# Kernel optimization log

Hardware: AMD Instinct MI355X
Metric: run time of the kernel (lower is better)

The kernel has to match this reference:

```python
import jax, jax.numpy as jnp
import numpy as np


def setup_inputs() -> dict:
    key = jax.random.key(0)
    ks = jax.random.split(key, 7)
    C = 256
    Cqk = C // 8  # 32
    B, D, H, W = 4, 16, 16, 16
    s_in = 1.0 / np.sqrt(C)  # conv1x1 fan_in = C
    return {
        "x": jax.random.normal(ks[0], (B, C, D, H, W), dtype=jnp.float32),
        "Wq": jax.random.uniform(ks[1], (Cqk, C), jnp.float32, -s_in, s_in),
        "bq": jax.random.uniform(ks[2], (Cqk,), jnp.float32, -s_in, s_in),
        "Wk": jax.random.uniform(ks[3], (Cqk, C), jnp.float32, -s_in, s_in),
        "bk": jax.random.uniform(ks[4], (Cqk,), jnp.float32, -s_in, s_in),
        "Wv": jax.random.uniform(ks[5], (C, C), jnp.float32, -s_in, s_in),
        "bv": jax.random.uniform(ks[6], (C,), jnp.float32, -s_in, s_in),
    }


def reference(x, Wq, bq, Wk, bk, Wv, bv):
    B, C, D, H, W = x.shape
    N = D * H * W
    xf = x.reshape(B, C, N)  # [B, C, N]
    # 1x1x1 convs == per-voxel GEMMs over the channel dim
    q = jnp.einsum('oc,bcn->bon', Wq, xf) + bq[None, :, None]  # [B, Cqk, N]
    k = jnp.einsum('oc,bcn->bon', Wk, xf) + bk[None, :, None]  # [B, Cqk, N]
    v = jnp.einsum('oc,bcn->bon', Wv, xf) + bv[None, :, None]  # [B, C, N]
    # attention[b, n, m] = softmax_m( q[:, n] . k[:, m] )
    scores = jnp.einsum('bcn,bcm->bnm', q, k)  # [B, N, N]
    attn = jax.nn.softmax(scores, axis=-1)
    # out = value @ attention^T  -> out[b, c, n] = sum_m v[b,c,m] * attn[b,n,m]
    out = jnp.einsum('bcm,bnm->bcn', v, attn)
    return x + out.reshape(B, C, D, H, W)
```

## Files before the change

### kernel.cpp

```cpp
#include <hip/hip_runtime.h>
#include <math.h>

#define B_   4
#define C_   256
#define CQK  32
#define N_   4096
#define TQ   64
#define TM   64
#define HITERS ((N_ / 2) / TM)
#define PSS  72
#define XT2  264
#define VOS  40

typedef __attribute__((ext_vector_type(8))) short short8;
typedef __attribute__((ext_vector_type(4))) short short4v;
typedef __attribute__((ext_vector_type(4))) float f32x4;
typedef __attribute__((ext_vector_type(2))) unsigned int uint2v;

#if __has_builtin(__builtin_amdgcn_exp2f)
#define EXP2F(x) __builtin_amdgcn_exp2f(x)
#else
#define EXP2F(x) exp2f(x)
#endif

__device__ __forceinline__ unsigned short f2bf(float f) {
    unsigned u = __builtin_bit_cast(unsigned, f);
    u += 0x7fffu + ((u >> 16) & 1u);
    return (unsigned short)(u >> 16);
}
__device__ __forceinline__ float bf2f(unsigned short s) {
    return __builtin_bit_cast(float, (unsigned)s << 16);
}
__device__ __forceinline__ unsigned pack2bf(float a, float b) {
    unsigned ua = __builtin_bit_cast(unsigned, a) + 0x8000u;
    unsigned ub = __builtin_bit_cast(unsigned, b) + 0x8000u;
#if __has_builtin(__builtin_amdgcn_perm)
    return __builtin_amdgcn_perm(ub, ua, 0x07060302u);
#else
    return (ua >> 16) | (ub & 0xffff0000u);
#endif
}

__global__ __launch_bounds__(256) void cvt_w(
    const float* __restrict__ Wq, const float* __restrict__ bq,
    const float* __restrict__ Wk, const float* __restrict__ bk,
    const float* __restrict__ Wv, const float* __restrict__ bv,
    unsigned short* __restrict__ wbf, float* __restrict__ biasf)
{
    const float LOG2E = 1.4426950408889634f;
    const int r = blockIdx.x;
    const int t = threadIdx.x;
    const float* src = (r < 32) ? (Wq + r * C_)
                     : (r < 64) ? (Wk + (r - 32) * C_)
                                : (Wv + (r - 64) * C_);
    const float scale = (r < 32) ? LOG2E : 1.0f;
    wbf[r * C_ + t] = f2bf(src[t] * scale);
    if (t == 0)
        biasf[r] = (r < 32) ? bq[r] * LOG2E : (r < 64) ? bk[r - 32] : bv[r - 64];
}

__global__ __launch_bounds__(256, 2) void proj_qkv(
    const float* __restrict__ x, const unsigned short* __restrict__ wbf,
    const float* __restrict__ biasf,
    unsigned short* __restrict__ qb, unsigned short* __restrict__ kb,
    unsigned short* __restrict__ vb)
{
    __shared__ __align__(16) unsigned short xT[32 * XT2];
    __shared__ __align__(16) unsigned short vout[256 * VOS];
    __shared__ __align__(16) unsigned short qks[32 * 72];

    const int t    = threadIdx.x;
    const int w    = t >> 6;
    const int lane = t & 63;
    const int quad = lane >> 4;
    const int c16  = lane & 15;
    const int n0   = blockIdx.x * 32;
    const int b    = blockIdx.y;

    {
        const int c0 = (t >> 3) * 8;
        const int nq = t & 7;
        f32x4 xv[8];
#pragma unroll
        for (int i = 0; i < 8; ++i)
            xv[i] = *(const f32x4*)&x[((size_t)(b * C_) + c0 + i) * N_ + n0 + 4 * nq];
#pragma unroll
        for (int j = 0; j < 4; ++j) {
            short8 pk;
#pragma unroll
            for (int i = 0; i < 8; ++i) pk[i] = (short)f2bf(xv[i][j]);
            *(short8*)&xT[(4 * nq + j) * XT2 + c0] = pk;
        }
    }
    __syncthreads();

    f32x4 acc[5][2];
#pragma unroll
    for (int i = 0; i < 5; ++i)
#pragma unroll
        for (int nt = 0; nt < 2; ++nt) acc[i][nt] = (f32x4){0.f, 0.f, 0.f, 0.f};

    const unsigned short* wr = wbf + (size_t)(80 * w + c16) * C_ + quad * 8;

#pragma unroll
    for (int ks = 0; ks < 8; ++ks) {
        short8 af[5], bf[2];
#pragma unroll
        for (int i = 0; i < 5; ++i)
            af[i] = *(const short8*)(wr + (size_t)(16 * i) * C_ + 32 * ks);
#pragma unroll
        for (int nt = 0; nt < 2; ++nt)
            bf[nt] = *(const short8*)&xT[(16 * nt + c16) * XT2 + ks * 32 + quad * 8];
#pragma unroll
        for (int i = 0; i < 5; ++i)
#pragma unroll
            for (int nt = 0; nt < 2; ++nt)
                acc[i][nt] = __builtin_amdgcn_mfma_f32_16x16x32_bf16(af[i], bf[nt], acc[i][nt], 0, 0, 0);
    }

#pragma unroll
    for (int i = 0; i < 5; ++i) {
        const int OT = 5 * w + i;
        const int obase = OT * 16 + 4 * quad;
        const f32x4 bv4 = *(const f32x4*)&biasf[obase];
#pragma unroll
        for (int nt = 0; nt < 2; ++nt) {
            const int n = 16 * nt + c16;
            float vals[4];
#pragma unroll
            for (int r = 0; r < 4; ++r) vals[r] = acc[i][nt][r] + bv4[r];
            if (OT >= 4) {
#pragma unroll
                for (int r = 0; r < 4; ++r)
                    vout[(obase + r - 64) * VOS + n] = f2bf(vals[r]);
            } else {
                const int col = (OT < 2 ? 0 : 32) + (OT & 1) * 16 + 4 * quad;
                short4v pk;
#pragma unroll
                for (int r = 0; r < 4; ++r) pk[r] = (short)f2bf(vals[r]);
                *(short4v*)&qks[n * 72 + col] = pk;
            }
        }
    }
    __syncthreads();

#pragma unroll
    for (int p = 0; p < 4; ++p) {
        const int c   = 64 * p + (t >> 2);
        const int seg = t & 3;
        const short8 vv = *(const short8*)&vout[c * VOS + seg * 8];
        *(short8*)(vb + ((size_t)(b * C_) + c) * N_ + n0 + seg * 8) = vv;
    }
    if (w < 2) {
        unsigned short* dst = w ? kb : qb;
        const int coff = w ? 32 : 0;
#pragma unroll
        for (int h = 0; h < 2; ++h) {
            const int n = 16 * h + (lane >> 2);
            const int c = (lane & 3) * 8;
            const short8 v = *(const short8*)&qks[n * 72 + coff + c];
            *(short8*)(dst + ((size_t)(b * N_) + n0 + n) * 32 + c) = v;
        }
    }
}

__global__ __launch_bounds__(512, 4) void attn_kernel(
    const unsigned short* __restrict__ qg,
    const unsigned short* __restrict__ kg,
    const unsigned short* __restrict__ vg,
    float* __restrict__ outp,
    unsigned short* __restrict__ Op1,
    float* __restrict__ lp)
{
    __shared__ __align__(16) unsigned short ks[TM * 40];
    __shared__ __align__(16) unsigned short vs[C_ * TM];
    __shared__ __align__(16) unsigned short ps[TQ * PSS];
    __shared__ float ls[4 * TQ];

    const int t    = threadIdx.x;
    const int w    = t >> 6;
    const int lane = t & 63;
    const int quad = lane >> 4;
    const int c16  = lane & 15;
    const int flat = blockIdx.x;
    const int half = flat & 1;
    const int b    = (flat >> 1) & 3;
    const int q0   = (flat >> 3) * TQ;
    const int kvb0 = half * (N_ / 2);
    const int f   = w & 3;
    const int qg_ = w >> 2;
    const int cs = w & 3;
    const int pg = w >> 2;

    const unsigned short* kbase = kg + (size_t)(b * N_) * 32;
    const unsigned short* vbase = vg + (size_t)(b * C_) * N_;

    short8 bq[2];
#pragma unroll
    for (int g = 0; g < 2; ++g)
        bq[g] = *(const short8*)(qg + ((size_t)(b * N_) + q0 + 16 * (2 * qg_ + g) + c16) * 32 + quad * 8);

    const int vc0 = t >> 3, vj = t & 7;
    const int kn = t >> 2, kseg = t & 3;

    short8 vpre[4], kpre;
#pragma unroll
    for (int p = 0; p < 4; ++p)
        vpre[p] = *(const short8*)(vbase + (size_t)(vc0 + 64 * p) * N_ + kvb0 + vj * 8);
    if (t < 256)
        kpre = *(const short8*)(kbase + (size_t)(kvb0 + kn) * 32 + kseg * 8);

    f32x4 O[4][2];
#pragma unroll
    for (int ct = 0; ct < 4; ++ct)
#pragma unroll
        for (int qt = 0; qt < 2; ++qt) O[ct][qt] = (f32x4){0.f, 0.f, 0.f, 0.f};

    float lacc[2] = {0.f, 0.f};

#pragma unroll 1
    for (int it = 0; it < HITERS; ++it) {
#pragma unroll
        for (int p = 0; p < 4; ++p) {
            const int c = vc0 + 64 * p;
            *(short8*)&vs[c * TM + 8 * (vj ^ (c & 7))] = vpre[p];
        }
        if (t < 256)
            *(short8*)&ks[kn * 40 + kseg * 8] = kpre;
        __syncthreads();

        const short8 ak = *(const short8*)&ks[(16 * f + c16) * 40 + quad * 8];
        const f32x4 z = {0.f, 0.f, 0.f, 0.f};
        f32x4 sf[2];
#pragma unroll
        for (int g = 0; g < 2; ++g)
            sf[g] = __builtin_amdgcn_mfma_f32_16x16x32_bf16(ak, bq[g], z, 0, 0, 0);

#pragma unroll
        for (int g = 0; g < 2; ++g) {
            float p[4];
#pragma unroll
            for (int r = 0; r < 4; ++r) p[r] = EXP2F(sf[g][r]);
            lacc[g] += (p[0] + p[1]) + (p[2] + p[3]);
            uint2v u;
            u.x = pack2bf(p[0], p[1]);
            u.y = pack2bf(p[2], p[3]);
            *(uint2v*)&ps[(16 * (2 * qg_ + g) + c16) * PSS + f * 16 + 4 * quad] = u;
        }
        __syncthreads();

        if (it < HITERS - 1) {
            const int kv0n = kvb0 + (it + 1) * TM;
#pragma unroll
            for (int p = 0; p < 4; ++p)
                vpre[p] = *(const short8*)(vbase + (size_t)(vc0 + 64 * p) * N_ + kv0n + vj * 8);
            if (t < 256)
                kpre = *(const short8*)(kbase + (size_t)(kv0n + kn) * 32 + kseg * 8);
        }

        short8 bp[2][2];
#pragma unroll
        for (int qt = 0; qt < 2; ++qt)
#pragma unroll
            for (int s = 0; s < 2; ++s)
                bp[qt][s] = *(const short8*)&ps[(32 * pg + 16 * qt + c16) * PSS + 32 * s + 8 * quad];
#pragma unroll
        for (int s = 0; s < 2; ++s)
#pragma unroll
            for (int ct = 0; ct < 4; ++ct) {
                const int c = 64 * cs + 16 * ct + c16;
                const short8 av = *(const short8*)&vs[c * TM + 8 * ((4 * s + quad) ^ (c & 7))];
#pragma unroll
                for (int qt = 0; qt < 2; ++qt)
                    O[ct][qt] = __builtin_amdgcn_mfma_f32_16x16x32_bf16(av, bp[qt][s], O[ct][qt], 0, 0, 0);
            }
        __syncthreads();
    }

#pragma unroll
    for (int g = 0; g < 2; ++g) {
        lacc[g] += __shfl_xor(lacc[g], 16);
        lacc[g] += __shfl_xor(lacc[g], 32);
    }
    if (quad == 0) {
#pragma unroll
        for (int g = 0; g < 2; ++g)
            ls[f * TQ + 16 * (2 * qg_ + g) + c16] = lacc[g];
    }
    __syncthreads();

    if (half == 0) {
        float* ob = outp + (size_t)(b * C_) * N_;
#pragma unroll
        for (int ct = 0; ct < 4; ++ct)
#pragma unroll
            for (int qt = 0; qt < 2; ++qt) {
                const int n = q0 + 32 * pg + 16 * qt + c16;
#pragma unroll
                for (int r = 0; r < 4; ++r) {
                    const int c = 64 * cs + 16 * ct + 4 * quad + r;
                    ob[(size_t)c * N_ + n] = O[ct][qt][r];
                }
            }
    } else {
        unsigned short* ob = Op1 + (size_t)(b * C_) * N_;
#pragma unroll
        for (int ct = 0; ct < 4; ++ct)
#pragma unroll
            for (int qt = 0; qt < 2; ++qt) {
                const int n = q0 + 32 * pg + 16 * qt + c16;
#pragma unroll
                for (int r = 0; r < 4; ++r) {
                    const int c = 64 * cs + 16 * ct + 4 * quad + r;
                    ob[(size_t)c * N_ + n] = f2bf(O[ct][qt][r]);
                }
            }
    }
    if (w == 0) {
        const int qq = lane;
        const float lv = ls[qq] + ls[TQ + qq] + ls[2 * TQ + qq] + ls[3 * TQ + qq];
        lp[(size_t)(half * B_ + b) * N_ + q0 + qq] = lv;
    }
}

__global__ __launch_bounds__(256) void combine_kernel(
    const float* __restrict__ x,
    const unsigned short* __restrict__ Op1,
    const float* __restrict__ lp,
    float* __restrict__ out)
{
    __shared__ float linv[1024];

    const int t  = threadIdx.x;
    const int n0 = blockIdx.x * 1024;
    const int c0 = blockIdx.y * 8;
    const int b  = blockIdx.z;

#pragma unroll
    for (int i = 0; i < 4; ++i) {
        const int n = n0 + t + 256 * i;
        const float l = lp[(size_t)b * N_ + n] + lp[(size_t)(B_ + b) * N_ + n];
        linv[t + 256 * i] = 1.0f / l;
    }
    __syncthreads();

#pragma unroll
    for (int cc = 0; cc < 8; ++cc) {
        const int c = c0 + cc;
        const size_t base = ((size_t)(b * C_) + c) * N_ + n0 + 4 * t;
        const f32x4 o0 = *(const f32x4*)&out[base];
        const short4v a1 = *(const short4v*)&Op1[base];
        const f32x4 xv = *(const f32x4*)&x[base];
        f32x4 o;
        o.x = xv.x + (o0.x + bf2f((unsigned short)a1[0])) * linv[4 * t + 0];
        o.y = xv.y + (o0.y + bf2f((unsigned short)a1[1])) * linv[4 * t + 1];
        o.z = xv.z + (o0.z + bf2f((unsigned short)a1[2])) * linv[4 * t + 2];
        o.w = xv.w + (o0.w + bf2f((unsigned short)a1[3])) * linv[4 * t + 3];
        *(f32x4*)&out[base] = o;
    }
}

extern "C" void kernel_launch(void* const* d_in, const int* in_sizes, int n_in,
                              void* d_out, int out_size, void* d_ws, size_t ws_size,
                              hipStream_t stream) {
    const float* x  = (const float*)d_in[0];
    const float* Wq = (const float*)d_in[1];
    const float* bq = (const float*)d_in[2];
    const float* Wk = (const float*)d_in[3];
    const float* bk = (const float*)d_in[4];
    const float* Wv = (const float*)d_in[5];
    const float* bv = (const float*)d_in[6];
    float* out = (float*)d_out;

    unsigned short* ws16 = (unsigned short*)d_ws;
    unsigned short* qb  = ws16;
    unsigned short* kb  = qb + (size_t)B_ * N_ * 32;
    unsigned short* vb  = kb + (size_t)B_ * N_ * 32;
    unsigned short* Op1 = vb + (size_t)B_ * C_ * N_;
    unsigned short* wbf = Op1 + (size_t)B_ * C_ * N_;
    float* biasf = (float*)(wbf + 320 * C_);
    float* lpp   = biasf + 320;

    cvt_w<<<dim3(320), 256, 0, stream>>>(Wq, bq, Wk, bk, Wv, bv, wbf, biasf);
    proj_qkv<<<dim3(N_ / 32, B_), 256, 0, stream>>>(x, wbf, biasf, qb, kb, vb);
    attn_kernel<<<dim3(512), 512, 0, stream>>>(qb, kb, vb, out, Op1, lpp);
    combine_kernel<<<dim3(4, 32, B_), 256, 0, stream>>>(x, Op1, lpp, out);
}
```

Baseline: 156.1 us.

## Double-buffer V tiles via direct global-to-LDS loads and keep K in registers

Replaces the register-staged V prefetch and LDS store with `global_load_lds` asynchronous copies into a double-buffered shared V tile, keeping the XOR swizzle by permuting global source addresses. K fragments are loaded straight from global into registers, which removes the K shared buffer and the barrier at the top of each iteration. The aim is to cut VGPR pressure, LDS store instructions and one sync per step while overlapping the next tile's load with the current MFMA work. In exchange, doubling the V buffer raises LDS use per block, which may lower the number of resident blocks per CU. Correctness also depends on the async LDS writes being waited on before the barrier.

```diff
diff --git a/kernel.cpp b/kernel.cpp
--- a/kernel.cpp
+++ b/kernel.cpp
@@ -9,6 +9,7 @@
 #define TM   64
 #define HITERS ((N_ / 2) / TM)
 #define PSS  72
+#define VSH  (C_ * TM)
 #define XT2  264
 #define VOS  40
 
@@ -22,6 +23,12 @@
 #else
 #define EXP2F(x) exp2f(x)
 #endif
+
+typedef const __attribute__((address_space(1))) unsigned int* gas1_t;
+typedef __attribute__((address_space(3))) unsigned int* las3_t;
+__device__ __forceinline__ void gload_lds16(const unsigned short* g, unsigned short* l) {
+    __builtin_amdgcn_global_load_lds((gas1_t)g, (las3_t)l, 16, 0, 0);
+}
 
 __device__ __forceinline__ unsigned short f2bf(float f) {
     unsigned u = __builtin_bit_cast(unsigned, f);
@@ -172,8 +179,7 @@
     unsigned short* __restrict__ Op1,
     float* __restrict__ lp)
 {
-    __shared__ __align__(16) unsigned short ks[TM * 40];
-    __shared__ __align__(16) unsigned short vs[C_ * TM];
+    __shared__ __align__(16) unsigned short vs[2 * VSH];
     __shared__ __align__(16) unsigned short ps[TQ * PSS];
     __shared__ float ls[4 * TQ];
 
@@ -200,15 +206,19 @@
     for (int g = 0; g < 2; ++g)
         bq[g] = *(const short8*)(qg + ((size_t)(b * N_) + q0 + 16 * (2 * qg_ + g) + c16) * 32 + quad * 8);
 
-    const int vc0 = t >> 3, vj = t & 7;
-    const int kn = t >> 2, kseg = t & 3;
-
-    short8 vpre[4], kpre;
-#pragma unroll
-    for (int p = 0; p < 4; ++p)
-        vpre[p] = *(const short8*)(vbase + (size_t)(vc0 + 64 * p) * N_ + kvb0 + vj * 8);
-    if (t < 256)
-        kpre = *(const short8*)(kbase + (size_t)(kvb0 + kn) * 32 + kseg * 8);
+    const int vrow  = lane >> 3;
+    const int vslot = lane & 7;
+
+    const size_t koff = (size_t)(16 * f + c16) * 32 + quad * 8;
+
+#pragma unroll
+    for (int p = 0; p < 4; ++p) {
+        const int c = 32 * w + 8 * p + vrow;
+        gload_lds16(vbase + (size_t)c * N_ + kvb0 + 8 * (vslot ^ (c & 7)),
+                    &vs[(32 * w + 8 * p) * TM]);
+    }
+    short8 akpre = *(const short8*)(kbase + (size_t)kvb0 * 32 + koff);
+    __syncthreads();
 
     f32x4 O[4][2];
 #pragma unroll
@@ -220,21 +230,14 @@
 
 #pragma unroll 1
     for (int it = 0; it < HITERS; ++it) {
-#pragma unroll
-        for (int p = 0; p < 4; ++p) {
-            const int c = vc0 + 64 * p;
-            *(short8*)&vs[c * TM + 8 * (vj ^ (c & 7))] = vpre[p];
-        }
-        if (t < 256)
-            *(short8*)&ks[kn * 40 + kseg * 8] = kpre;
-        __syncthreads();
-
-        const short8 ak = *(const short8*)&ks[(16 * f + c16) * 40 + quad * 8];
+        const int cur = it & 1;
+        const int nxt = cur ^ 1;
+
         const f32x4 z = {0.f, 0.f, 0.f, 0.f};
         f32x4 sf[2];
 #pragma unroll
         for (int g = 0; g < 2; ++g)
-            sf[g] = __builtin_amdgcn_mfma_f32_16x16x32_bf16(ak, bq[g], z, 0, 0, 0);
+            sf[g] = __builtin_amdgcn_mfma_f32_16x16x32_bf16(akpre, bq[g], z, 0, 0, 0);
 
 #pragma unroll
         for (int g = 0; g < 2; ++g) {
@@ -249,13 +252,15 @@
         }
         __syncthreads();
 
-        if (it < HITERS - 1) {
+        if (it + 1 < HITERS) {
             const int kv0n = kvb0 + (it + 1) * TM;
 #pragma unroll
-            for (int p = 0; p < 4; ++p)
-                vpre[p] = *(const short8*)(vbase + (size_t)(vc0 + 64 * p) * N_ + kv0n + vj * 8);
-            if (t < 256)
-                kpre = *(const short8*)(kbase + (size_t)(kv0n + kn) * 32 + kseg * 8);
+            for (int p = 0; p < 4; ++p) {
+                const int c = 32 * w + 8 * p + vrow;
+                gload_lds16(vbase + (size_t)c * N_ + kv0n + 8 * (vslot ^ (c & 7)),
+                            &vs[nxt * VSH + (32 * w + 8 * p) * TM]);
+            }
+            akpre = *(const short8*)(kbase + (size_t)kv0n * 32 + koff);
         }
 
         short8 bp[2][2];
@@ -269,7 +274,7 @@
 #pragma unroll
             for (int ct = 0; ct < 4; ++ct) {
                 const int c = 64 * cs + 16 * ct + c16;
-                const short8 av = *(const short8*)&vs[c * TM + 8 * ((4 * s + quad) ^ (c & 7))];
+                const short8 av = *(const short8*)&vs[cur * VSH + c * TM + 8 * ((4 * s + quad) ^ (c & 7))];
 #pragma unroll
                 for (int qt = 0; qt < 2; ++qt)
                     O[ct][qt] = __builtin_amdgcn_mfma_f32_16x16x32_bf16(av, bp[qt][s], O[ct][qt], 0, 0, 0);
```

Result: faster. 145.0 us (-7.1%).
